# Kernel optimization log

Hardware: AMD Instinct MI355X
Metric: run time of the kernel (lower is better)

The kernel has to match this reference:

```python
import jax, jax.numpy as jnp
import numpy as np

LATENT = 256
C = 512            # channels == window_size
STEP = C // 2      # 256
N_SAMPLES = 32768
N_FRAMES = N_SAMPLES // STEP   # 128
IMP = 4096         # impulse samples
B, E = 4, 64
EPS = 1e-8


def unit_norm(x, axis=-1):
    return x / (jnp.linalg.norm(x, axis=axis, keepdims=True) + EPS)


def hamming(n):
    # torch.hamming_window default (periodic=True)
    return (0.54 - 0.46 * jnp.cos(2.0 * jnp.pi * jnp.arange(n) / n)).astype(jnp.float32)


def layer_norm(x, g, b):
    mu = x.mean(-1, keepdims=True)
    var = x.var(-1, keepdims=True)
    return (x - mu) / jnp.sqrt(var + 1e-5) * g + b


def mlp(x, Ws, bs, g, bt):
    # LinearOutputStack: 3 hidden (linear -> LayerNorm -> leaky_relu) + output linear
    for j in range(3):
        x = x @ Ws[j] + bs[j]
        x = layer_norm(x, g[j], bt[j])
        x = jax.nn.leaky_relu(x, 0.2)
    return x @ Ws[3] + bs[3]


def _forward(embedding, impulse, W_def, b_def,
             Ws_imp, bs_imp, g_imp, bt_imp,
             Ws_lat, bs_lat, g_lat, bt_lat,
             Ws_out, bs_out, g_out, bt_out,
             W_w, b_w, W_b, b_b, W_l, b_l):
    Bq, Eq, _ = embedding.shape
    # shape deformations: latent -> (C, n_frames), unit-normed over channel dim
    deform = (embedding @ W_def + b_def).reshape(Bq, Eq, C, N_FRAMES)
    deform = unit_norm(deform, axis=2)
    deform = deform.transpose(0, 1, 3, 2)           # (B,E,T,C)
    weights = deform @ W_w + b_w                    # (B,E,T,C)
    biases = deform @ W_b + b_b                     # (B,E,T,C)
    leak = 0.1 + jax.nn.sigmoid(deform @ W_l + b_l) * 0.98  # (B,E,T,1)

    # window the impulse: frames of size C with hop STEP
    padded = jnp.pad(impulse, ((0, 0), (0, 0), (0, STEP)))
    starts = jnp.arange(IMP // STEP) * STEP
    idx = starts[:, None] + jnp.arange(C)[None, :]
    windowed = padded[..., idx]                     # (B,E,16,C)
    norms = jnp.linalg.norm(windowed, axis=-1, keepdims=True)
    emb = mlp(windowed, Ws_imp, bs_imp, g_imp, bt_imp)
    emb = unit_norm(emb) * norms                    # (B,E,16,C)
    # pad with zeros to n_frames: adding zero == original i < n_impulse_frames guard
    emb_pad = jnp.pad(emb, ((0, 0), (0, 0), (0, N_FRAMES - emb.shape[2]), (0, 0)))

    ham = hamming(C)

    xs = (weights.transpose(2, 0, 1, 3),
          biases.transpose(2, 0, 1, 3),
          leak.transpose(2, 0, 1, 3),
          emb_pad.transpose(2, 0, 1, 3))

    def step(h, x):
        w, b, lk, e = x
        h = h + e
        cn = jnp.linalg.norm(h, axis=-1, keepdims=True)
        h = h * w + b
        h = unit_norm(h) * cn
        ol = mlp(h, Ws_lat, bs_lat, g_lat, bt_lat)
        ol = unit_norm(ol) * (cn * lk)
        on = jnp.linalg.norm(ol, axis=-1, keepdims=True)
        h = h - ol
        h = unit_norm(h) * (cn - on)
        of = mlp(ol, Ws_out, bs_out, g_out, bt_out)
        of = of * ham
        of = unit_norm(of) * on
        return h, of

    h0 = jnp.zeros((Bq, Eq, C), dtype=embedding.dtype)
    _, frames = jax.lax.scan(step, h0, xs)          # (T,B,E,C)
    frames = frames.transpose(1, 2, 0, 3)           # (B,E,T,C)

    # overlap-add at hop STEP, trim to n_samples
    L = (N_FRAMES - 1) * STEP + C
    oa_idx = jnp.arange(N_FRAMES)[:, None] * STEP + jnp.arange(C)[None, :]
    out = jnp.zeros((Bq, Eq, L), dtype=embedding.dtype)
    out = out.at[:, :, oa_idx].add(frames)
    return out[..., :N_SAMPLES]


def setup_inputs() -> dict:
    key = jax.random.key(0)
    ks = jax.random.split(key, 24)
    s = 0.02
    d = {
        'embedding': jax.random.normal(ks[0], (B, E, LATENT), jnp.float32),
        'impulse': jax.random.normal(ks[1], (B, E, IMP), jnp.float32),
        'W_def': jax.random.normal(ks[2], (LATENT, C * N_FRAMES), jnp.float32) * s,
        'b_def': jnp.zeros((C * N_FRAMES,), jnp.float32),
        'W_w': jax.random.normal(ks[3], (C, C), jnp.float32) * s,
        'b_w': jnp.zeros((C,), jnp.float32),
        'W_b': jax.random.normal(ks[4], (C, C), jnp.float32) * s,
        'b_b': jnp.zeros((C,), jnp.float32),
        'W_l': jax.random.normal(ks[5], (C, 1), jnp.float32) * s,
        'b_l': jnp.zeros((1,), jnp.float32),
    }
    for name, k in (('imp', ks[6]), ('lat', ks[7]), ('out', ks[8])):
        d['Ws_' + name] = jax.random.normal(k, (4, C, C), jnp.float32) * s
        d['bs_' + name] = jnp.zeros((4, C), jnp.float32)
        d['g_' + name] = jnp.ones((3, C), jnp.float32)
        d['bt_' + name] = jnp.zeros((3, C), jnp.float32)
    return d


def reference(embedding, impulse, W_def, b_def,
              Ws_imp, bs_imp, g_imp, bt_imp,
              Ws_lat, bs_lat, g_lat, bt_lat,
              Ws_out, bs_out, g_out, bt_out,
              W_w, b_w, W_b, b_b, W_l, b_l):
    return _forward(embedding, impulse, W_def, b_def,
                    Ws_imp, bs_imp, g_imp, bt_imp,
                    Ws_lat, bs_lat, g_lat, bt_lat,
                    Ws_out, bs_out, g_out, bt_out,
                    W_w, b_w, W_b, b_b, W_l, b_l)
```

## Files before the change

kernel.cpp:

```cpp
#include <hip/hip_runtime.h>
#include <math.h>

#define NB 4
#define NE 64
#define BE 256
#define LAT 256
#define NC 512
#define NT 128
#define NDEF 65536
#define NIMP 4096
#define NF 16
#define EPSN 1e-8f
#define SPB 4
#define NSCAN 64

typedef unsigned short ushort8 __attribute__((ext_vector_type(8)));
typedef short short8v __attribute__((ext_vector_type(8)));
typedef float f32x4 __attribute__((ext_vector_type(4)));

__device__ __forceinline__ unsigned short f2bf(float f) {
  const unsigned u = __float_as_uint(f);
  return (unsigned short)((u + 0x7FFFu + ((u >> 16) & 1u)) >> 16);
}

__device__ __forceinline__ void bar_nodrain() {
  asm volatile("s_waitcnt lgkmcnt(0)" ::: "memory");
  __builtin_amdgcn_s_barrier();
  __builtin_amdgcn_sched_barrier(0);
}

template <int NR>
__device__ __forceinline__ void blk_reduce1(const float* v, float* out,
                                            float* red) {
  const int tid = threadIdx.x, wave = tid >> 6, lane = tid & 63;
  float s[NR];
#pragma unroll
  for (int i = 0; i < NR; ++i) s[i] = v[i];
#pragma unroll
  for (int off = 32; off; off >>= 1) {
#pragma unroll
    for (int i = 0; i < NR; ++i) s[i] += __shfl_down(s[i], off);
  }
  if (lane == 0) {
#pragma unroll
    for (int i = 0; i < NR; ++i) red[wave * NR + i] = s[i];
  }
  bar_nodrain();
#pragma unroll
  for (int i = 0; i < NR; ++i) {
    float a = 0.f;
#pragma unroll
    for (int w = 0; w < 8; ++w) a += red[w * NR + i];
    out[i] = a;
  }
}

__global__ __launch_bounds__(64) void k_cvt(const float* __restrict__ W,
                                            unsigned short* __restrict__ Wmf) {
  const int lane = threadIdx.x;
  const int gg = blockIdx.x;
  const int p = gg & 3;
  const int kt = (gg >> 2) & 15;
  const int wv = (gg >> 6) & 7;
  const int layer = gg >> 9;
  const int col = wv * 64 + p * 16 + (lane & 15);
  const int k0 = kt * 32 + (lane >> 4) * 8;
  ushort8 o;
#pragma unroll
  for (int j = 0; j < 8; ++j)
    o[j] = f2bf(W[((size_t)layer * NC + k0 + j) * NC + col]);
  *reinterpret_cast<ushort8*>(Wmf + ((size_t)gg * 64 + lane) * 8) = o;
}

__global__ __launch_bounds__(256) void k_deform(
    const float* __restrict__ emb, const float* __restrict__ Wd,
    const float* __restrict__ bd, float* __restrict__ deform) {
  __shared__ float As[32][LAT];
  const int tid = threadIdx.x;
  const int c = blockIdx.x * 256 + tid;
  const int m0 = blockIdx.y * 32;
  for (int i = 0; i < 32; ++i) As[i][tid] = emb[(m0 + i) * LAT + tid];
  __syncthreads();
  float acc[32];
#pragma unroll
  for (int i = 0; i < 32; ++i) acc[i] = 0.f;
  for (int k = 0; k < LAT; k += 4) {
    const float w0 = Wd[(size_t)(k + 0) * NDEF + c];
    const float w1 = Wd[(size_t)(k + 1) * NDEF + c];
    const float w2 = Wd[(size_t)(k + 2) * NDEF + c];
    const float w3 = Wd[(size_t)(k + 3) * NDEF + c];
#pragma unroll
    for (int i = 0; i < 32; ++i) {
      const float4 a = *reinterpret_cast<const float4*>(&As[i][k]);
      acc[i] = fmaf(a.x, w0, acc[i]);
      acc[i] = fmaf(a.y, w1, acc[i]);
      acc[i] = fmaf(a.z, w2, acc[i]);
      acc[i] = fmaf(a.w, w3, acc[i]);
    }
  }
  const float bv = bd[c];
  for (int i = 0; i < 32; ++i)
    deform[(size_t)(m0 + i) * NDEF + c] = acc[i] + bv;
}

__global__ __launch_bounds__(512) void k_wb(
    const float* __restrict__ deform, const unsigned short* __restrict__ Wmf2,
    const float* __restrict__ bw, const float* __restrict__ bb,
    const float* __restrict__ Wl, const float* __restrict__ bl,
    float* __restrict__ weights, float* __restrict__ biases,
    float* __restrict__ leak) {
  __shared__ float xs[16][NC];
  __shared__ __align__(16) unsigned short A_lds[16 * NC];
  __shared__ float rno[16], lks[16];
  const int tid = threadIdx.x;
  const int wave = tid >> 6, lane = tid & 63;
  const int be = blockIdx.x >> 3;
  const int t0 = (blockIdx.x & 7) * 16;
  const float* dbase = deform + (size_t)be * NDEF;
  for (int i = 0; i < 16; ++i)
    xs[i][tid] = dbase[(size_t)tid * NT + t0 + i];
  __syncthreads();
  for (int f = wave; f < 16; f += 8) {
    float s = 0.f;
#pragma unroll
    for (int j = 0; j < 8; ++j) {
      const float v = xs[f][lane + 64 * j];
      s = fmaf(v, v, s);
    }
#pragma unroll
    for (int off = 32; off; off >>= 1) s += __shfl_down(s, off);
    if (lane == 0) rno[f] = sqrtf(s);
  }
  __syncthreads();
  {
    char* ab = (char*)A_lds;
#pragma unroll
    for (int i = 0; i < 16; ++i) {
      const float xv = xs[i][tid] / (rno[i] + EPSN);
      xs[i][tid] = xv;
      *(unsigned short*)(ab + i * 1024 + ((tid * 2) ^ ((i & 7) << 4))) =
          f2bf(xv);
    }
  }
  __syncthreads();
  for (int f = wave; f < 16; f += 8) {
    float s = 0.f;
#pragma unroll
    for (int j = 0; j < 8; ++j)
      s = fmaf(xs[f][lane + 64 * j], Wl[lane + 64 * j], s);
#pragma unroll
    for (int off = 32; off; off >>= 1) s += __shfl_down(s, off);
    if (lane == 0) lks[f] = s;
  }
  __syncthreads();
  if (tid < 16) {
    const float v = lks[tid] + bl[0];
    leak[(size_t)be * NT + t0 + tid] = 0.1f + 0.98f / (1.f + expf(-v));
  }
  const int arow = lane & 15;
  const int kgrp = lane >> 4;
  const int r0 = kgrp * 4;
  const int abase = arow * (NC * 2);
  const int axor = (arow & 7) << 4;
  const int akoff = kgrp * 16;
  float bwv[4], bbv[4];
#pragma unroll
  for (int p = 0; p < 4; ++p) {
    const int cp = wave * 64 + p * 16 + (lane & 15);
    bwv[p] = bw[cp];
    bbv[p] = bb[cp];
  }
  const unsigned short* wfrag = Wmf2 + (size_t)wave * 32768 + lane * 8;
  f32x4 accw[4], accb[4];
#pragma unroll
  for (int p = 0; p < 4; ++p) {
    accw[p] = (f32x4){0.f, 0.f, 0.f, 0.f};
    accb[p] = (f32x4){0.f, 0.f, 0.f, 0.f};
  }
#pragma unroll
  for (int kt = 0; kt < 16; ++kt) {
    const short8v a = *(const short8v*)((const char*)A_lds + abase +
                                        (((kt * 64) + akoff) ^ axor));
#pragma unroll
    for (int p = 0; p < 4; ++p) {
      const short8v b0 = *(const short8v*)(wfrag + (kt * 4 + p) * 512);
      accw[p] = __builtin_amdgcn_mfma_f32_16x16x32_bf16(a, b0, accw[p], 0, 0, 0);
      const short8v b1 =
          *(const short8v*)(wfrag + (size_t)262144 + (kt * 4 + p) * 512);
      accb[p] = __builtin_amdgcn_mfma_f32_16x16x32_bf16(a, b1, accb[p], 0, 0, 0);
    }
  }
#pragma unroll
  for (int q = 0; q < 4; ++q) {
    const int row = r0 + q;
#pragma unroll
    for (int p = 0; p < 4; ++p) {
      const int cp = wave * 64 + p * 16 + (lane & 15);
      const size_t o = ((size_t)be * NT + t0 + row) * NC + cp;
      weights[o] = accw[p][q] + bwv[p];
      biases[o] = accb[p][q] + bbv[p];
    }
  }
}

__device__ __forceinline__ void tile_gemm16(const float (*xs)[NC],
                                            const float* __restrict__ W,
                                            int tid, float acc[16]) {
#pragma unroll
  for (int i = 0; i < 16; ++i) acc[i] = 0.f;
  for (int k = 0; k < NC; k += 4) {
    const float w0 = W[(size_t)(k + 0) * NC + tid];
    const float w1 = W[(size_t)(k + 1) * NC + tid];
    const float w2 = W[(size_t)(k + 2) * NC + tid];
    const float w3 = W[(size_t)(k + 3) * NC + tid];
#pragma unroll
    for (int i = 0; i < 16; ++i) {
      const float4 a = *reinterpret_cast<const float4*>(&xs[i][k]);
      acc[i] = fmaf(a.x, w0, acc[i]);
      acc[i] = fmaf(a.y, w1, acc[i]);
      acc[i] = fmaf(a.z, w2, acc[i]);
      acc[i] = fmaf(a.w, w3, acc[i]);
    }
  }
}

__device__ __forceinline__ void ln_leaky16(float (*xs)[NC],
                                           const float* __restrict__ g,
                                           const float* __restrict__ bt,
                                           int layer, int tid, float* mu_s,
                                           float* rs_s) {
  const int wave = tid >> 6, lane = tid & 63;
  for (int f = wave; f < 16; f += 8) {
    float s = 0.f, s2 = 0.f;
#pragma unroll
    for (int j = 0; j < 8; ++j) {
      const float v = xs[f][lane + 64 * j];
      s += v;
      s2 = fmaf(v, v, s2);
    }
#pragma unroll
    for (int off = 32; off; off >>= 1) {
      s += __shfl_down(s, off);
      s2 += __shfl_down(s2, off);
    }
    if (lane == 0) {
      const float mu = s * (1.f / NC);
      mu_s[f] = mu;
      rs_s[f] = rsqrtf(s2 * (1.f / NC) - mu * mu + 1e-5f);
    }
  }
  __syncthreads();
  const float gv = g[layer * NC + tid], btv = bt[layer * NC + tid];
#pragma unroll
  for (int i = 0; i < 16; ++i) {
    const float y = (xs[i][tid] - mu_s[i]) * rs_s[i] * gv + btv;
    xs[i][tid] = y > 0.f ? y : 0.2f * y;
  }
  __syncthreads();
}

__global__ __launch_bounds__(512) void k_imp(
    const float* __restrict__ impulse, const float* __restrict__ Ws,
    const float* __restrict__ bs, const float* __restrict__ g,
    const float* __restrict__ bt, float* __restrict__ embo) {
  __shared__ float xs[16][NC];
  __shared__ float wno[16], mu_s[16], rs_s[16], ono[16];
  const int tid = threadIdx.x;
  const int wave = tid >> 6, lane = tid & 63;
  const int be = blockIdx.x;
  const float* ib = impulse + (size_t)be * NIMP;
  for (int f = 0; f < 16; ++f) {
    const int s = f * 256 + tid;
    xs[f][tid] = (s < NIMP) ? ib[s] : 0.f;
  }
  __syncthreads();
  for (int f = wave; f < 16; f += 8) {
    float s = 0.f;
#pragma unroll
    for (int j = 0; j < 8; ++j) {
      const float v = xs[f][lane + 64 * j];
      s = fmaf(v, v, s);
    }
#pragma unroll
    for (int off = 32; off; off >>= 1) s += __shfl_down(s, off);
    if (lane == 0) wno[f] = sqrtf(s);
  }
  __syncthreads();
  float acc[16];
  for (int layer = 0; layer < 4; ++layer) {
    tile_gemm16(xs, Ws + (size_t)layer * NC * NC, tid, acc);
    __syncthreads();
    const float bv = bs[layer * NC + tid];
#pragma unroll
    for (int i = 0; i < 16; ++i) xs[i][tid] = acc[i] + bv;
    __syncthreads();
    if (layer < 3) ln_leaky16(xs, g, bt, layer, tid, mu_s, rs_s);
  }
  for (int f = wave; f < 16; f += 8) {
    float s = 0.f;
#pragma unroll
    for (int j = 0; j < 8; ++j) {
      const float v = xs[f][lane + 64 * j];
      s = fmaf(v, v, s);
    }
#pragma unroll
    for (int off = 32; off; off >>= 1) s += __shfl_down(s, off);
    if (lane == 0) ono[f] = sqrtf(s);
  }
  __syncthreads();
  for (int f = 0; f < 16; ++f)
    embo[((size_t)be * NF + f) * NC + tid] =
        xs[f][tid] / (ono[f] + EPSN) * wno[f];
}

__global__ __launch_bounds__(512) void k_scan(
    const float* __restrict__ weights, const float* __restrict__ biases,
    const float* __restrict__ leak, const float* __restrict__ embw,
    const unsigned short* __restrict__ Wmf, const float* __restrict__ bs,
    const float* __restrict__ g, const float* __restrict__ bt,
    float* __restrict__ olb, float* __restrict__ onb) {
  __shared__ __align__(16) unsigned short A_lds[16 * NC];
  __shared__ __align__(16) unsigned short B_lds[8][4][2048];
  __shared__ float ol_lds[SPB][NC];
  __shared__ float redA[64];
  __shared__ float redB[32];
  __shared__ float st1[8][SPB], st2[8][SPB];
  __shared__ float lk_lds[SPB][NT];

  const int tid = threadIdx.x;
  const int wave = tid >> 6, lane = tid & 63;
  const int seq0 = blockIdx.x * SPB;

  {
    const int r = tid >> 7, tt = tid & 127;
    lk_lds[r][tt] = leak[(size_t)(seq0 + r) * NT + tt];
  }
  {
    unsigned* z = (unsigned*)(A_lds + SPB * NC);
    for (int i = tid; i < (16 - SPB) * NC / 2; i += 512) z[i] = 0u;
  }

  const int arow = lane & 15;
  const int kgrp = lane >> 4;
  const int abase = arow * (NC * 2);
  const int axor = (arow & 7) << 4;
  const int akoff = kgrp * 16;
  const bool crow = (kgrp == 0);

  float bsv[4][4], gv[3][4], btv[3][4];
#pragma unroll
  for (int p = 0; p < 4; ++p) {
    const int cp = wave * 64 + p * 16 + (lane & 15);
#pragma unroll
    for (int l = 0; l < 4; ++l) bsv[l][p] = bs[l * NC + cp];
#pragma unroll
    for (int l = 0; l < 3; ++l) {
      gv[l][p] = g[l * NC + cp];
      btv[l][p] = bt[l * NC + cp];
    }
  }
  const unsigned short* wfrag = Wmf + (size_t)wave * 32768 + lane * 8;

  auto issue_chunk = [&](int cc) {
    const int layer = cc >> 4, kt = cc & 15, slot = cc & 3;
#pragma unroll
    for (int p = 0; p < 4; ++p) {
      __builtin_amdgcn_global_load_lds(
          (const unsigned int*)(wfrag + (size_t)layer * 262144 +
                                (kt * 4 + p) * 512),
          (unsigned int*)&B_lds[wave][slot][p * 512], 16, 0, 0);
    }
  };

  float wpre[SPB], bpre[SPB], epre[SPB];
#pragma unroll
  for (int r = 0; r < SPB; ++r) {
    const size_t o = ((size_t)(seq0 + r) * NT) * NC + tid;
    wpre[r] = weights[o];
    bpre[r] = biases[o];
    epre[r] = embw[((size_t)(seq0 + r) * NF) * NC + tid];
  }

  __syncthreads();

  issue_chunk(0);
  issue_chunk(1);
  issue_chunk(2);

  float h[SPB], cn[SPB];
#pragma unroll
  for (int r = 0; r < SPB; ++r) { h[r] = 0.f; cn[r] = 0.f; }

#pragma unroll 1
  for (int t = 0; t < NT; ++t) {
    float hw[SPB];
    if (t < NF) {
#pragma unroll
      for (int r = 0; r < SPB; ++r) h[r] += epre[r];
      if (t + 1 < NF) {
#pragma unroll
        for (int r = 0; r < SPB; ++r)
          epre[r] = embw[((size_t)(seq0 + r) * NF + t + 1) * NC + tid];
      }
      float v8[8], s8[8];
#pragma unroll
      for (int r = 0; r < SPB; ++r) {
        hw[r] = fmaf(h[r], wpre[r], bpre[r]);
        v8[r] = h[r] * h[r];
        v8[SPB + r] = hw[r] * hw[r];
      }
      blk_reduce1<8>(v8, s8, redA);
#pragma unroll
      for (int r = 0; r < SPB; ++r) {
        cn[r] = sqrtf(s8[r]);
        h[r] = hw[r] * (cn[r] / (sqrtf(s8[SPB + r]) + EPSN));
      }
    } else {
      float v4[SPB], s4[SPB];
#pragma unroll
      for (int r = 0; r < SPB; ++r) {
        hw[r] = fmaf(h[r], wpre[r], bpre[r]);
        v4[r] = hw[r] * hw[r];
      }
      blk_reduce1<SPB>(v4, s4, redA);
#pragma unroll
      for (int r = 0; r < SPB; ++r)
        h[r] = hw[r] * (cn[r] / (sqrtf(s4[r]) + EPSN));
    }
    if (t + 1 < NT) {
#pragma unroll
      for (int r = 0; r < SPB; ++r) {
        const size_t o = ((size_t)(seq0 + r) * NT + t + 1) * NC + tid;
        wpre[r] = weights[o];
        bpre[r] = biases[o];
      }
    }
    {
      char* ab = (char*)A_lds;
#pragma unroll
      for (int r = 0; r < SPB; ++r)
        *(unsigned short*)(ab + r * 1024 + ((tid * 2) ^ ((r & 7) << 4))) =
            f2bf(h[r]);
    }
    bar_nodrain();

#pragma unroll 1
    for (int layer = 0; layer < 4; ++layer) {
      f32x4 acc[4];
#pragma unroll
      for (int p = 0; p < 4; ++p) acc[p] = (f32x4){0.f, 0.f, 0.f, 0.f};
#pragma unroll
      for (int kt = 0; kt < 16; ++kt) {
        asm volatile("s_waitcnt vmcnt(8)" ::: "memory");
        const short8v a = *(const short8v*)((const char*)A_lds + abase +
                                            (((kt * 64) + akoff) ^ axor));
        const int slot = kt & 3;
#pragma unroll
        for (int p = 0; p < 4; ++p) {
          const short8v b =
              *(const short8v*)((const char*)&B_lds[wave][slot][0] + p * 1024 +
                                lane * 16);
          acc[p] =
              __builtin_amdgcn_mfma_f32_16x16x32_bf16(a, b, acc[p], 0, 0, 0);
        }
        issue_chunk((layer * 16 + kt + 3) & 63);
      }

      if (layer < 3) {
        float s1[SPB], s2[SPB];
#pragma unroll
        for (int q = 0; q < SPB; ++q) { s1[q] = 0.f; s2[q] = 0.f; }
#pragma unroll
        for (int p = 0; p < 4; ++p) {
#pragma unroll
          for (int q = 0; q < SPB; ++q) {
            const float y = acc[p][q] + bsv[layer][p];
            acc[p][q] = y;
            s1[q] += y;
            s2[q] = fmaf(y, y, s2[q]);
          }
        }
#pragma unroll
        for (int off = 1; off < 16; off <<= 1) {
#pragma unroll
          for (int q = 0; q < SPB; ++q) {
            s1[q] += __shfl_xor(s1[q], off);
            s2[q] += __shfl_xor(s2[q], off);
          }
        }
        if (lane == 0) {
#pragma unroll
          for (int q = 0; q < SPB; ++q) {
            st1[wave][q] = s1[q];
            st2[wave][q] = s2[q];
          }
        }
        bar_nodrain();
        float mu[SPB], rs[SPB];
#pragma unroll
        for (int q = 0; q < SPB; ++q) {
          float a1 = 0.f, a2 = 0.f;
#pragma unroll
          for (int w = 0; w < 8; ++w) {
            a1 += st1[w][q];
            a2 += st2[w][q];
          }
          mu[q] = a1 * (1.f / NC);
          rs[q] = rsqrtf(a2 * (1.f / NC) - mu[q] * mu[q] + 1e-5f);
        }
        if (crow) {
          char* ab = (char*)A_lds;
#pragma unroll
          for (int q = 0; q < SPB; ++q) {
#pragma unroll
            for (int p = 0; p < 4; ++p) {
              float y = (acc[p][q] - mu[q]) * rs[q] * gv[layer][p] +
                        btv[layer][p];
              y = y > 0.f ? y : 0.2f * y;
              const int cp = wave * 64 + p * 16 + (lane & 15);
              *(unsigned short*)(ab + q * 1024 +
                                 ((cp * 2) ^ ((q & 7) << 4))) = f2bf(y);
            }
          }
        }
        bar_nodrain();
      } else {
        float s2[SPB];
#pragma unroll
        for (int q = 0; q < SPB; ++q) s2[q] = 0.f;
#pragma unroll
        for (int p = 0; p < 4; ++p) {
#pragma unroll
          for (int q = 0; q < SPB; ++q) {
            const float y = acc[p][q] + bsv[3][p];
            acc[p][q] = y;
            s2[q] = fmaf(y, y, s2[q]);
          }
        }
#pragma unroll
        for (int off = 1; off < 16; off <<= 1) {
#pragma unroll
          for (int q = 0; q < SPB; ++q) s2[q] += __shfl_xor(s2[q], off);
        }
        if (lane == 0) {
#pragma unroll
          for (int q = 0; q < SPB; ++q) st2[wave][q] = s2[q];
        }
        if (crow) {
#pragma unroll
          for (int q = 0; q < SPB; ++q) {
#pragma unroll
            for (int p = 0; p < 4; ++p)
              ol_lds[q][wave * 64 + p * 16 + (lane & 15)] = acc[p][q];
          }
        }
        bar_nodrain();
        float sc[SPB], on[SPB];
#pragma unroll
        for (int r = 0; r < SPB; ++r) {
          float a2 = 0.f;
#pragma unroll
          for (int w = 0; w < 8; ++w) a2 += st2[w][r];
          const float no = sqrtf(a2);
          sc[r] = cn[r] * lk_lds[r][t] / (no + EPSN);
          on[r] = no * sc[r];
        }
        if (tid < SPB) onb[(size_t)(seq0 + tid) * NT + t] = on[tid];
        float v4[SPB], s4[SPB];
#pragma unroll
        for (int r = 0; r < SPB; ++r) {
          const float olv = ol_lds[r][tid] * sc[r];
          olb[((size_t)(seq0 + r) * NT + t) * NC + tid] = olv;
          h[r] -= olv;
          v4[r] = h[r] * h[r];
        }
        blk_reduce1<SPB>(v4, s4, redB);
#pragma unroll
        for (int r = 0; r < SPB; ++r) {
          h[r] *= (cn[r] - on[r]) / (sqrtf(s4[r]) + EPSN);
          cn[r] = fabsf(cn[r] - on[r]);
        }
      }
    }
  }
}

__global__ __launch_bounds__(512) void k_out(
    const float* __restrict__ olb, const float* __restrict__ onb,
    const unsigned short* __restrict__ Wmf, const float* __restrict__ bs,
    const float* __restrict__ g, const float* __restrict__ bt,
    float* __restrict__ ofb) {
  __shared__ __align__(16) unsigned short A_lds[16 * NC];
  __shared__ float st1[8][16], st2[8][16];
  __shared__ float on_l[16];
  const int tid = threadIdx.x;
  const int wave = tid >> 6, lane = tid & 63;
  const int m0 = blockIdx.x * 16;
  const int arow = lane & 15;
  const int kgrp = lane >> 4;
  const int r0 = kgrp * 4;
  const int abase = arow * (NC * 2);
  const int axor = (arow & 7) << 4;
  const int akoff = kgrp * 16;

  float bsv[4][4], gv[3][4], btv[3][4], hamv[4];
#pragma unroll
  for (int p = 0; p < 4; ++p) {
    const int cp = wave * 64 + p * 16 + (lane & 15);
#pragma unroll
    for (int l = 0; l < 4; ++l) bsv[l][p] = bs[l * NC + cp];
#pragma unroll
    for (int l = 0; l < 3; ++l) {
      gv[l][p] = g[l * NC + cp];
      btv[l][p] = bt[l * NC + cp];
    }
    hamv[p] =
        0.54f - 0.46f * cosf(6.283185307179586f * (float)cp / (float)NC);
  }
  if (tid < 16) on_l[tid] = onb[m0 + tid];
  {
    char* ab = (char*)A_lds;
    for (int i = 0; i < 16; ++i) {
      const float v = olb[(size_t)(m0 + i) * NC + tid];
      *(unsigned short*)(ab + i * 1024 + ((tid * 2) ^ ((i & 7) << 4))) =
          f2bf(v);
    }
  }
  __syncthreads();

  const unsigned short* wfrag = Wmf + (size_t)wave * 32768 + lane * 8;

#pragma unroll 1
  for (int layer = 0; layer < 4; ++layer) {
    f32x4 acc[4];
#pragma unroll
    for (int p = 0; p < 4; ++p) acc[p] = (f32x4){0.f, 0.f, 0.f, 0.f};
#pragma unroll
    for (int kt = 0; kt < 16; ++kt) {
      const short8v a = *(const short8v*)((const char*)A_lds + abase +
                                          (((kt * 64) + akoff) ^ axor));
#pragma unroll
      for (int p = 0; p < 4; ++p) {
        const short8v b = *(const short8v*)(wfrag + (size_t)layer * 262144 +
                                            (kt * 4 + p) * 512);
        acc[p] = __builtin_amdgcn_mfma_f32_16x16x32_bf16(a, b, acc[p], 0, 0, 0);
      }
    }
    if (layer < 3) {
      float s1[4], s2[4];
#pragma unroll
      for (int q = 0; q < 4; ++q) { s1[q] = 0.f; s2[q] = 0.f; }
#pragma unroll
      for (int p = 0; p < 4; ++p) {
#pragma unroll
        for (int q = 0; q < 4; ++q) {
          const float y = acc[p][q] + bsv[layer][p];
          acc[p][q] = y;
          s1[q] += y;
          s2[q] = fmaf(y, y, s2[q]);
        }
      }
#pragma unroll
      for (int off = 1; off < 16; off <<= 1) {
#pragma unroll
        for (int q = 0; q < 4; ++q) {
          s1[q] += __shfl_xor(s1[q], off);
          s2[q] += __shfl_xor(s2[q], off);
        }
      }
      if ((lane & 15) == 0) {
#pragma unroll
        for (int q = 0; q < 4; ++q) {
          st1[wave][r0 + q] = s1[q];
          st2[wave][r0 + q] = s2[q];
        }
      }
      __syncthreads();
      char* ab = (char*)A_lds;
#pragma unroll
      for (int q = 0; q < 4; ++q) {
        const int row = r0 + q;
        float a1 = 0.f, a2 = 0.f;
#pragma unroll
        for (int w = 0; w < 8; ++w) {
          a1 += st1[w][row];
          a2 += st2[w][row];
        }
        const float mu = a1 * (1.f / NC);
        const float rs = rsqrtf(a2 * (1.f / NC) - mu * mu + 1e-5f);
#pragma unroll
        for (int p = 0; p < 4; ++p) {
          float y = (acc[p][q] - mu) * rs * gv[layer][p] + btv[layer][p];
          y = y > 0.f ? y : 0.2f * y;
          const int cp = wave * 64 + p * 16 + (lane & 15);
          *(unsigned short*)(ab + row * 1024 +
                             ((cp * 2) ^ ((row & 7) << 4))) = f2bf(y);
        }
      }
      __syncthreads();
    } else {
      float s2[4];
#pragma unroll
      for (int q = 0; q < 4; ++q) s2[q] = 0.f;
#pragma unroll
      for (int p = 0; p < 4; ++p) {
#pragma unroll
        for (int q = 0; q < 4; ++q) {
          float y = (acc[p][q] + bsv[3][p]) * hamv[p];
          acc[p][q] = y;
          s2[q] = fmaf(y, y, s2[q]);
        }
      }
#pragma unroll
      for (int off = 1; off < 16; off <<= 1) {
#pragma unroll
        for (int q = 0; q < 4; ++q) s2[q] += __shfl_xor(s2[q], off);
      }
      if ((lane & 15) == 0) {
#pragma unroll
        for (int q = 0; q < 4; ++q) st2[wave][r0 + q] = s2[q];
      }
      __syncthreads();
#pragma unroll
      for (int q = 0; q < 4; ++q) {
        const int row = r0 + q;
        float a2 = 0.f;
#pragma unroll
        for (int w = 0; w < 8; ++w) a2 += st2[w][row];
        const float inv = on_l[row] / (sqrtf(a2) + EPSN);
#pragma unroll
        for (int p = 0; p < 4; ++p) {
          const int cp = wave * 64 + p * 16 + (lane & 15);
          ofb[(size_t)(m0 + row) * NC + cp] = acc[p][q] * inv;
        }
      }
    }
  }
}

__global__ __launch_bounds__(256) void k_oa(const float* __restrict__ ofb,
                                            float* __restrict__ out) {
  const int idx = blockIdx.x * 256 + threadIdx.x;
  if (idx >= BE * 32768) return;
  const int be = idx >> 15;
  const int s = idx & 32767;
  const int t1 = s >> 8;
  float v = ofb[((size_t)be * NT + t1) * NC + (s - (t1 << 8))];
  if (t1 >= 1)
    v += ofb[((size_t)be * NT + (t1 - 1)) * NC + (s - ((t1 - 1) << 8))];
  out[idx] = v;
}

extern "C" void kernel_launch(void* const* d_in, const int* in_sizes, int n_in,
                              void* d_out, int out_size, void* d_ws,
                              size_t ws_size, hipStream_t stream) {
  const float* embedding = (const float*)d_in[0];
  const float* impulse = (const float*)d_in[1];
  const float* W_def = (const float*)d_in[2];
  const float* b_def = (const float*)d_in[3];
  const float* W_w = (const float*)d_in[4];
  const float* b_w = (const float*)d_in[5];
  const float* W_b = (const float*)d_in[6];
  const float* b_b = (const float*)d_in[7];
  const float* W_l = (const float*)d_in[8];
  const float* b_l = (const float*)d_in[9];
  const float* Ws_imp = (const float*)d_in[10];
  const float* bs_imp = (const float*)d_in[11];
  const float* g_imp = (const float*)d_in[12];
  const float* bt_imp = (const float*)d_in[13];
  const float* Ws_lat = (const float*)d_in[14];
  const float* bs_lat = (const float*)d_in[15];
  const float* g_lat = (const float*)d_in[16];
  const float* bt_lat = (const float*)d_in[17];
  const float* Ws_out = (const float*)d_in[18];
  const float* bs_out = (const float*)d_in[19];
  const float* g_out = (const float*)d_in[20];
  const float* bt_out = (const float*)d_in[21];
  float* out = (float*)d_out;

  float* ws = (float*)d_ws;
  float* deform = ws;
  float* weights = deform + 16777216;
  float* biases = weights + 16777216;
  float* leakb = biases + 16777216;
  float* embw = leakb + 32768;
  float* onb = embw + 2097152;
  unsigned short* wmf = (unsigned short*)(onb + 32768);
  unsigned short* wmf_out = wmf + 1048576;
  unsigned short* wmf_wb = wmf_out + 1048576;
  float* olb = deform;
  float* ofb = weights;

  k_cvt<<<2048, 64, 0, stream>>>(Ws_lat, wmf);
  k_cvt<<<2048, 64, 0, stream>>>(Ws_out, wmf_out);
  k_cvt<<<512, 64, 0, stream>>>(W_w, wmf_wb);
  k_cvt<<<512, 64, 0, stream>>>(W_b, wmf_wb + 262144);
  k_deform<<<dim3(256, 8), 256, 0, stream>>>(embedding, W_def, b_def, deform);
  k_wb<<<2048, 512, 0, stream>>>(deform, wmf_wb, b_w, b_b, W_l, b_l,
                                 weights, biases, leakb);
  k_imp<<<256, 512, 0, stream>>>(impulse, Ws_imp, bs_imp, g_imp, bt_imp, embw);
  k_scan<<<NSCAN, 512, 0, stream>>>(weights, biases, leakb, embw, wmf, bs_lat,
                                    g_lat, bt_lat, olb, onb);
  k_out<<<2048, 512, 0, stream>>>(olb, onb, wmf_out, bs_out, g_out, bt_out,
                                  ofb);
  k_oa<<<32768, 256, 0, stream>>>(ofb, out);
}
```

Baseline: 4.474 ms.

## Fuse overlap-add into output MLP via atomics and hoist scan prefetches

Removes the separate overlap-add kernel and its intermediate frame buffer: the output MLP kernel now atomically adds each windowed frame directly into the zeroed output, and a small zeroing kernel is added. In the recurrent scan, the loads of next-step weights, biases and impulse embeddings are moved before the block reduction so their latency overlaps the reduction. The atomics add contention and make summation order nondeterministic, and the output must be zeroed every call.

```diff
diff --git a/kernel.cpp b/kernel.cpp
--- a/kernel.cpp
+++ b/kernel.cpp
@@ -13,6 +13,7 @@
 #define EPSN 1e-8f
 #define SPB 4
 #define NSCAN 64
+#define NSAMP 32768
 
 typedef unsigned short ushort8 __attribute__((ext_vector_type(8)));
 typedef short short8v __attribute__((ext_vector_type(8)));
@@ -397,11 +398,6 @@
     if (t < NF) {
 #pragma unroll
       for (int r = 0; r < SPB; ++r) h[r] += epre[r];
-      if (t + 1 < NF) {
-#pragma unroll
-        for (int r = 0; r < SPB; ++r)
-          epre[r] = embw[((size_t)(seq0 + r) * NF + t + 1) * NC + tid];
-      }
       float v8[8], s8[8];
 #pragma unroll
       for (int r = 0; r < SPB; ++r) {
@@ -409,6 +405,19 @@
         v8[r] = h[r] * h[r];
         v8[SPB + r] = hw[r] * hw[r];
       }
+      if (t + 1 < NF) {
+#pragma unroll
+        for (int r = 0; r < SPB; ++r)
+          epre[r] = embw[((size_t)(seq0 + r) * NF + t + 1) * NC + tid];
+      }
+      if (t + 1 < NT) {
+#pragma unroll
+        for (int r = 0; r < SPB; ++r) {
+          const size_t o = ((size_t)(seq0 + r) * NT + t + 1) * NC + tid;
+          wpre[r] = weights[o];
+          bpre[r] = biases[o];
+        }
+      }
       blk_reduce1<8>(v8, s8, redA);
 #pragma unroll
       for (int r = 0; r < SPB; ++r) {
@@ -422,18 +431,18 @@
         hw[r] = fmaf(h[r], wpre[r], bpre[r]);
         v4[r] = hw[r] * hw[r];
       }
+      if (t + 1 < NT) {
+#pragma unroll
+        for (int r = 0; r < SPB; ++r) {
+          const size_t o = ((size_t)(seq0 + r) * NT + t + 1) * NC + tid;
+          wpre[r] = weights[o];
+          bpre[r] = biases[o];
+        }
+      }
       blk_reduce1<SPB>(v4, s4, redA);
 #pragma unroll
       for (int r = 0; r < SPB; ++r)
         h[r] = hw[r] * (cn[r] / (sqrtf(s4[r]) + EPSN));
-    }
-    if (t + 1 < NT) {
-#pragma unroll
-      for (int r = 0; r < SPB; ++r) {
-        const size_t o = ((size_t)(seq0 + r) * NT + t + 1) * NC + tid;
-        wpre[r] = weights[o];
-        bpre[r] = biases[o];
-      }
     }
     {
       char* ab = (char*)A_lds;
@@ -585,11 +594,15 @@
   }
 }
 
+__global__ __launch_bounds__(1024) void k_zero(float* __restrict__ out) {
+  out[(size_t)blockIdx.x * 1024 + threadIdx.x] = 0.f;
+}
+
 __global__ __launch_bounds__(512) void k_out(
     const float* __restrict__ olb, const float* __restrict__ onb,
     const unsigned short* __restrict__ Wmf, const float* __restrict__ bs,
     const float* __restrict__ g, const float* __restrict__ bt,
-    float* __restrict__ ofb) {
+    float* __restrict__ out) {
   __shared__ __align__(16) unsigned short A_lds[16 * NC];
   __shared__ float st1[8][16], st2[8][16];
   __shared__ float on_l[16];
@@ -724,6 +737,9 @@
 #pragma unroll
       for (int q = 0; q < 4; ++q) {
         const int row = r0 + q;
+        const int gr = m0 + row;
+        const int be = gr >> 7;
+        const int tt = gr & 127;
         float a2 = 0.f;
 #pragma unroll
         for (int w = 0; w < 8; ++w) a2 += st2[w][row];
@@ -731,24 +747,13 @@
 #pragma unroll
         for (int p = 0; p < 4; ++p) {
           const int cp = wave * 64 + p * 16 + (lane & 15);
-          ofb[(size_t)(m0 + row) * NC + cp] = acc[p][q] * inv;
-        }
-      }
-    }
-  }
-}
-
-__global__ __launch_bounds__(256) void k_oa(const float* __restrict__ ofb,
-                                            float* __restrict__ out) {
-  const int idx = blockIdx.x * 256 + threadIdx.x;
-  if (idx >= BE * 32768) return;
-  const int be = idx >> 15;
-  const int s = idx & 32767;
-  const int t1 = s >> 8;
-  float v = ofb[((size_t)be * NT + t1) * NC + (s - (t1 << 8))];
-  if (t1 >= 1)
-    v += ofb[((size_t)be * NT + (t1 - 1)) * NC + (s - ((t1 - 1) << 8))];
-  out[idx] = v;
+          const int s = tt * 256 + cp;
+          if (s < NSAMP)
+            atomicAdd(&out[(size_t)be * NSAMP + s], acc[p][q] * inv);
+        }
+      }
+    }
+  }
 }
 
 extern "C" void kernel_launch(void* const* d_in, const int* in_sizes, int n_in,
@@ -789,7 +794,6 @@
   unsigned short* wmf_out = wmf + 1048576;
   unsigned short* wmf_wb = wmf_out + 1048576;
   float* olb = deform;
-  float* ofb = weights;
 
   k_cvt<<<2048, 64, 0, stream>>>(Ws_lat, wmf);
   k_cvt<<<2048, 64, 0, stream>>>(Ws_out, wmf_out);
@@ -799,9 +803,9 @@
   k_wb<<<2048, 512, 0, stream>>>(deform, wmf_wb, b_w, b_b, W_l, b_l,
                                  weights, biases, leakb);
   k_imp<<<256, 512, 0, stream>>>(impulse, Ws_imp, bs_imp, g_imp, bt_imp, embw);
+  k_zero<<<(BE * NSAMP) / 1024, 1024, 0, stream>>>(out);
   k_scan<<<NSCAN, 512, 0, stream>>>(weights, biases, leakb, embw, wmf, bs_lat,
                                     g_lat, bt_lat, olb, onb);
   k_out<<<2048, 512, 0, stream>>>(olb, onb, wmf_out, bs_out, g_out, bt_out,
-                                  ofb);
-  k_oa<<<32768, 256, 0, stream>>>(ofb, out);
-}
+                                  out);
+}
```

After: 4.312 ms. 3.6% less time.
